# Kernel optimization log

Hardware: AMD Instinct MI355X
Metric: run time of the kernel (lower is better)

The kernel has to match this reference:

```python
import jax, jax.numpy as jnp
import numpy as np

D_MODEL = 1024
N_EXPERTS = 8
TOP_K = 2
D_FF = 4 * D_MODEL
BATCH, SEQ = 4, 2048


def setup_inputs() -> dict:
    key = jax.random.key(0)
    ks = jax.random.split(key, 7)
    s = 0.02
    return {
        "x": jax.random.normal(ks[0], (BATCH, SEQ, D_MODEL), dtype=jnp.float32),
        "Wg": jax.random.normal(ks[1], (D_MODEL, N_EXPERTS), dtype=jnp.float32) * s,
        "bg": jnp.zeros((N_EXPERTS,), dtype=jnp.float32),
        "W1": jax.random.normal(ks[2], (N_EXPERTS, D_MODEL, D_FF), dtype=jnp.float32) * s,
        "b1": jnp.zeros((N_EXPERTS, D_FF), dtype=jnp.float32),
        "W2": jax.random.normal(ks[3], (N_EXPERTS, D_FF, D_MODEL), dtype=jnp.float32) * s,
        "b2": jnp.zeros((N_EXPERTS, D_MODEL), dtype=jnp.float32),
    }


def reference(x, Wg, bg, W1, b1, W2, b2):
    B, S, D = x.shape
    T = B * S
    xf = x.reshape(T, D)  # [T, d_model]

    # Gating: top-k over softmax probabilities
    gate_logits = xf @ Wg + bg                      # [T, E]
    probs = jax.nn.softmax(gate_logits, axis=-1)
    weights, indices = jax.lax.top_k(probs, TOP_K)  # [T, K] each

    # Dense combine weights c[t, e] = sum_k weights[t,k] * (indices[t,k]==e)
    E = Wg.shape[1]
    c = jnp.zeros((T, E), dtype=x.dtype).at[jnp.arange(T)[:, None], indices].add(weights)

    # All-expert FFN as batched GEMMs (same math as masked per-expert loop)
    h = jnp.einsum('td,edf->etf', xf, W1) + b1[:, None, :]   # [E, T, d_ff]
    a = jax.nn.gelu(h, approximate=False)
    y = jnp.einsum('etf,efd->etd', a, W2) + b2[:, None, :]   # [E, T, d_model]

    out = jnp.einsum('te,etd->td', c, y).reshape(B, S, D)
    return out, gate_logits
```

## Files before the change

kernel.cpp:

```cpp
#include <hip/hip_runtime.h>
#include <hip/hip_bf16.h>
#include <math.h>

#define D_MODEL 1024
#define N_EXP   8
#define D_FF    4096
#define T_TOK   8192
#define NPAIR   (T_TOK * 2)
#define CAP_ROWS (NPAIR + N_EXP * 128)
#define MAX_TILES (CAP_ROWS / 128)

typedef __attribute__((ext_vector_type(4)))  float  f32x4;
typedef __attribute__((ext_vector_type(16))) float  f32x16;
typedef __attribute__((ext_vector_type(8)))  __bf16 bf16x8;
typedef __attribute__((ext_vector_type(4)))  __bf16 bf16x4;

#define OFF_W1T   0
#define OFF_W2T   67108864
#define OFF_H     134217728
#define OFF_XR    276824064
#define OFF_META  312475648
#define M_PAIREXP 0
#define M_PAIRW   65536
#define M_ROW2P   131072
#define M_COUNTS  200704
#define M_PADST   200736
#define M_CURSOR  200768
#define M_T2E     201792
#define M_TROW    202336

__device__ __forceinline__ void async_copy16(const void* g, void* s) {
  __builtin_amdgcn_global_load_lds(
      (const __attribute__((address_space(1))) void*)g,
      (__attribute__((address_space(3))) void*)s, 16, 0, 0);
}

__device__ __forceinline__ float gelu_fast(float v) {
  float u = 1.5957691216057308f * (v + 0.044715f * v * v * v);
  return v * __builtin_amdgcn_rcpf(1.f + __expf(-u));
}

__global__ void k_gate(const float* __restrict__ x, const float* __restrict__ Wg,
                       const float* __restrict__ bg, float* __restrict__ logits_out,
                       int* __restrict__ pairExpert, float* __restrict__ pairW) {
  const int t    = blockIdx.x * 4 + (threadIdx.x >> 6);
  const int lane = threadIdx.x & 63;
  const float* xp = x + (size_t)t * D_MODEL;
  float acc[8];
#pragma unroll
  for (int e = 0; e < 8; e++) acc[e] = 0.f;
#pragma unroll
  for (int i = 0; i < 16; i++) {
    int d = i * 64 + lane;
    float xv = xp[d];
    const float4* wr = (const float4*)(Wg + d * 8);
    float4 w0 = wr[0], w1 = wr[1];
    acc[0] += xv * w0.x; acc[1] += xv * w0.y; acc[2] += xv * w0.z; acc[3] += xv * w0.w;
    acc[4] += xv * w1.x; acc[5] += xv * w1.y; acc[6] += xv * w1.z; acc[7] += xv * w1.w;
  }
#pragma unroll
  for (int e = 0; e < 8; e++)
#pragma unroll
    for (int off = 32; off > 0; off >>= 1) acc[e] += __shfl_down(acc[e], off);
  if (lane == 0) {
    float l[8];
#pragma unroll
    for (int e = 0; e < 8; e++) { l[e] = acc[e] + bg[e]; logits_out[t * 8 + e] = l[e]; }
    float m = l[0];
#pragma unroll
    for (int e = 1; e < 8; e++) m = fmaxf(m, l[e]);
    float p[8], s = 0.f;
#pragma unroll
    for (int e = 0; e < 8; e++) { p[e] = expf(l[e] - m); s += p[e]; }
    float inv = 1.0f / s;
    int i1 = 0;
#pragma unroll
    for (int e = 1; e < 8; e++) if (l[e] > l[i1]) i1 = e;
    int i2 = (i1 == 0) ? 1 : 0;
#pragma unroll
    for (int e = 0; e < 8; e++) if (e != i1 && l[e] > l[i2]) i2 = e;
    pairExpert[t * 2 + 0] = i1; pairW[t * 2 + 0] = p[i1] * inv;
    pairExpert[t * 2 + 1] = i2; pairW[t * 2 + 1] = p[i2] * inv;
  }
}

__global__ void k_init(int* __restrict__ row2pair) {
  int i = blockIdx.x * 256 + threadIdx.x;
  if (i < CAP_ROWS) row2pair[i] = -1;
}

__global__ void k_offsets(const int* __restrict__ pairExpert, int* __restrict__ counts,
                          int* __restrict__ padStart, int* __restrict__ cursor,
                          int* __restrict__ t2e, int* __restrict__ trow) {
  __shared__ int hist[8];
  int tid = threadIdx.x;
  if (tid < 8) hist[tid] = 0;
  __syncthreads();
  for (int i = tid; i < NPAIR; i += 256) atomicAdd(&hist[pairExpert[i]], 1);
  __syncthreads();
  if (tid == 0) {
    int run = 0, nt = 0;
    for (int e = 0; e < 8; e++) {
      counts[e] = hist[e]; padStart[e] = run; cursor[e * 32] = 0;
      int tiles = (hist[e] + 127) >> 7;
      for (int i = 0; i < tiles; i++) { t2e[nt] = e; trow[nt] = run + i * 128; nt++; }
      run += tiles * 128;
    }
    for (; nt < MAX_TILES; nt++) t2e[nt] = -1;
  }
}

__global__ void k_place(const int* __restrict__ pairExpert, const int* __restrict__ padStart,
                        int* __restrict__ cursor, int* __restrict__ row2pair) {
  int p = blockIdx.x * 256 + threadIdx.x;
  if (p >= NPAIR) return;
  int e = pairExpert[p];
  int r = atomicAdd(&cursor[e * 32], 1);
  row2pair[padStart[e] + r] = p;
}

__global__ void k_gather(const float* __restrict__ x, const int* __restrict__ row2pair,
                         __bf16* __restrict__ XR) {
  int row = blockIdx.x;
  int pair = row2pair[row];
  int c = threadIdx.x * 4;
  __bf16* dst = XR + (size_t)row * D_MODEL + c;
  if (pair < 0) {
    bf16x4 z = {(__bf16)0.f, (__bf16)0.f, (__bf16)0.f, (__bf16)0.f};
    *(bf16x4*)dst = z;
  } else {
    int t = pair >> 1;
    float4 v = *(const float4*)(x + (size_t)t * D_MODEL + c);
    bf16x4 o = {(__bf16)v.x, (__bf16)v.y, (__bf16)v.z, (__bf16)v.w};
    *(bf16x4*)dst = o;
  }
}

__global__ void k_convT(const float* __restrict__ in, __bf16* __restrict__ out,
                        int R, int C) {
  __shared__ __bf16 tile[64][68];
  int e = blockIdx.z;
  const float* ip = in + (size_t)e * R * C + (size_t)(blockIdx.y * 64) * C + blockIdx.x * 64;
  __bf16* op = out + (size_t)e * R * C + (size_t)(blockIdx.x * 64) * R + blockIdx.y * 64;
#pragma unroll
  for (int it = 0; it < 4; it++) {
    int idx = it * 1024 + threadIdx.x * 4;
    int lr = idx >> 6, lc = idx & 63;
    float4 v = *(const float4*)(ip + (size_t)lr * C + lc);
    bf16x4 o = {(__bf16)v.x, (__bf16)v.y, (__bf16)v.z, (__bf16)v.w};
    *(bf16x4*)&tile[lr][lc] = o;
  }
  __syncthreads();
#pragma unroll
  for (int it = 0; it < 4; it++) {
    int idx = it * 1024 + threadIdx.x * 4;
    int lc = idx >> 6, lr = idx & 63;
    bf16x4 o = {tile[lr + 0][lc], tile[lr + 1][lc], tile[lr + 2][lc], tile[lr + 3][lc]};
    *(bf16x4*)(op + (size_t)lc * R + lr) = o;
  }
}


#define STG(SW, T)                                                         \
  do {                                                                     \
    size_t _ko = (size_t)(T) * 64;                                         \
    async_copy16(srcA0 + _ko, (SW) + w * 1024);                            \
    async_copy16(srcA1 + _ko, (SW) + (w + 4) * 1024);                      \
    async_copy16(srcB0 + _ko, (SW) + 8192 + w * 1024);                     \
    async_copy16(srcB1 + _ko, (SW) + 8192 + (w + 4) * 1024);               \
  } while (0)

#define LDF(SR)                                                            \
  do {                                                                     \
    _Pragma("unroll")                                                      \
    for (int mi = 0; mi < 2; mi++)                                         \
      _Pragma("unroll")                                                    \
      for (int kc = 0; kc < 2; kc++)                                       \
        Af[mi][kc] = *(const bf16x8*)((SR) + (wm + mi * 32 + l31) * 64 + (aoff ^ (kc << 5))); \
    _Pragma("unroll")                                                      \
    for (int nj = 0; nj < 2; nj++)                                         \
      _Pragma("unroll")                                                    \
      for (int kc = 0; kc < 2; kc++)                                       \
        Bf[nj][kc] = *(const bf16x8*)((SR) + 8192 + (wn + nj * 32 + l31) * 64 + (aoff ^ (kc << 5))); \
  } while (0)

#define MFM                                                                \
  do {                                                                     \
    __builtin_amdgcn_s_setprio(1);                                         \
    _Pragma("unroll")                                                      \
    for (int kc = 0; kc < 2; kc++)                                         \
      _Pragma("unroll")                                                    \
      for (int mi = 0; mi < 2; mi++)                                       \
        _Pragma("unroll")                                                  \
        for (int nj = 0; nj < 2; nj++)                                     \
          acc[mi][nj] = __builtin_amdgcn_mfma_f32_32x32x16_bf16(           \
              Af[mi][kc], Bf[nj][kc], acc[mi][nj], 0, 0, 0);               \
    __builtin_amdgcn_s_setprio(0);                                         \
  } while (0)

#define ENDW(N)                                                            \
  do {                                                                     \
    __builtin_amdgcn_sched_barrier(0);                                     \
    asm volatile("s_waitcnt vmcnt(" #N ")" ::: "memory");                  \
    __builtin_amdgcn_s_barrier();                                          \
    asm volatile("" ::: "memory");                                         \
  } while (0)

#define BODY(SR, SW, T) \
  do { bf16x8 Af[2][2], Bf[2][2]; STG(SW, T); LDF(SR); MFM; ENDW(4); } while (0)
#define BODY_N0(SR) \
  do { bf16x8 Af[2][2], Bf[2][2]; LDF(SR); MFM; ENDW(0); } while (0)
#define BODY_LAST(SR) \
  do { bf16x8 Af[2][2], Bf[2][2]; LDF(SR); MFM; } while (0)

__global__ __launch_bounds__(256, 3) void k_gemm1(
    const __bf16* __restrict__ XR, const __bf16* __restrict__ W1T,
    const float* __restrict__ b1, __bf16* __restrict__ H,
    const int* __restrict__ t2e, const int* __restrict__ trow) {
  __shared__ __align__(16) char lds[3][16384];
  const int bid = blockIdx.x;
  const int q = bid >> 8, w8 = bid & 255;
  const int nb = w8 >> 3, mt = q * 8 + (w8 & 7);
  const int e = t2e[mt];
  if (e < 0) return;
  const int rowBase = trow[mt];
  const int n0 = nb * 128;

  const int tid = threadIdx.x;
  const int l = tid & 63, w = tid >> 6;
  const int wm = (w >> 1) * 64, wn = (w & 1) * 64;
  const int l31 = l & 31, half = l >> 5;
  const int rsub = l >> 2;
  const int sg = (l & 3) ^ ((l >> 3) & 3);
  const int aoff = ((half ^ ((l >> 1) & 3)) << 4);

  const char* srcA0 = (const char*)(XR + (size_t)(rowBase + 16 * w + rsub) * D_MODEL) + sg * 16;
  const char* srcA1 = srcA0 + (size_t)64 * D_MODEL * 2;
  const __bf16* Bb = W1T + (size_t)e * D_FF * D_MODEL + (size_t)n0 * D_MODEL;
  const char* srcB0 = (const char*)(Bb + (size_t)(16 * w + rsub) * D_MODEL) + sg * 16;
  const char* srcB1 = srcB0 + (size_t)64 * D_MODEL * 2;

  f32x16 acc[2][2];
#pragma unroll
  for (int i = 0; i < 2; i++)
#pragma unroll
    for (int j = 0; j < 2; j++) acc[i][j] = (f32x16)(0.f);

  char* s0 = &lds[0][0]; char* s1 = &lds[1][0]; char* s2 = &lds[2][0];

  STG(s0, 0);
  STG(s1, 1);
  ENDW(4);

#pragma unroll 1
  for (int g = 0; g < 10; g++) {
    int t = 3 * g;
    BODY(s0, s2, t + 2);
    BODY(s1, s0, t + 3);
    BODY(s2, s1, t + 4);
  }
  BODY_N0(s0);
  BODY_LAST(s1);

  int colv[2]; float biasv[2];
#pragma unroll
  for (int nj = 0; nj < 2; nj++) {
    colv[nj] = n0 + wn + nj * 32 + l31;
    biasv[nj] = b1[e * D_FF + colv[nj]];
  }
#pragma unroll
  for (int mi = 0; mi < 2; mi++)
#pragma unroll
    for (int r = 0; r < 16; r++) {
      size_t row = (size_t)rowBase + wm + mi * 32 + (r & 3) + 8 * (r >> 2) + 4 * half;
#pragma unroll
      for (int nj = 0; nj < 2; nj++)
        H[row * D_FF + colv[nj]] = (__bf16)gelu_fast(acc[mi][nj][r] + biasv[nj]);
    }
}

__global__ __launch_bounds__(256, 3) void k_gemm2(
    const __bf16* __restrict__ H, const __bf16* __restrict__ W2T,
    const float* __restrict__ b2, float* __restrict__ out,
    const int* __restrict__ row2pair, const float* __restrict__ pairW,
    const int* __restrict__ t2e, const int* __restrict__ trow) {
  __shared__ __align__(16) char lds[3][16384];
  const int bid = blockIdx.x;
  const int q = bid >> 6, w8 = bid & 63;
  const int nb = w8 >> 3, mt = q * 8 + (w8 & 7);
  const int e = t2e[mt];
  if (e < 0) return;
  const int rowBase = trow[mt];
  const int n0 = nb * 128;

  const int tid = threadIdx.x;
  const int l = tid & 63, w = tid >> 6;
  const int wm = (w >> 1) * 64, wn = (w & 1) * 64;
  const int l31 = l & 31, half = l >> 5;
  const int rsub = l >> 2;
  const int sg = (l & 3) ^ ((l >> 3) & 3);
  const int aoff = ((half ^ ((l >> 1) & 3)) << 4);

  const char* srcA0 = (const char*)(H + (size_t)(rowBase + 16 * w + rsub) * D_FF) + sg * 16;
  const char* srcA1 = srcA0 + (size_t)64 * D_FF * 2;
  const __bf16* Bb = W2T + (size_t)e * D_MODEL * D_FF + (size_t)n0 * D_FF;
  const char* srcB0 = (const char*)(Bb + (size_t)(16 * w + rsub) * D_FF) + sg * 16;
  const char* srcB1 = srcB0 + (size_t)64 * D_FF * 2;

  f32x16 acc[2][2];
#pragma unroll
  for (int i = 0; i < 2; i++)
#pragma unroll
    for (int j = 0; j < 2; j++) acc[i][j] = (f32x16)(0.f);

  char* s0 = &lds[0][0]; char* s1 = &lds[1][0]; char* s2 = &lds[2][0];

  STG(s0, 0);
  STG(s1, 1);
  ENDW(4);

#pragma unroll 1
  for (int g = 0; g < 42; g++) {
    int t = 3 * g;
    BODY(s0, s2, t + 2);
    BODY(s1, s0, t + 3);
    BODY(s2, s1, t + 4);
  }
  BODY_N0(s0);
  BODY_LAST(s1);

  int colv[2]; float biasv[2];
#pragma unroll
  for (int nj = 0; nj < 2; nj++) {
    colv[nj] = n0 + wn + nj * 32 + l31;
    biasv[nj] = b2[e * D_MODEL + colv[nj]];
  }
#pragma unroll
  for (int mi = 0; mi < 2; mi++)
#pragma unroll
    for (int r = 0; r < 16; r++) {
      int row = rowBase + wm + mi * 32 + (r & 3) + 8 * (r >> 2) + 4 * half;
      int pair = row2pair[row];
      if (pair < 0) continue;
      float pw = pairW[pair];
      size_t tok = (size_t)(pair >> 1);
#pragma unroll
      for (int nj = 0; nj < 2; nj++)
        atomicAdd(out + tok * D_MODEL + colv[nj], pw * (acc[mi][nj][r] + biasv[nj]));
    }
}

extern "C" void kernel_launch(void* const* d_in, const int* in_sizes, int n_in,
                              void* d_out, int out_size, void* d_ws, size_t ws_size,
                              hipStream_t stream) {
  const float* x  = (const float*)d_in[0];
  const float* Wg = (const float*)d_in[1];
  const float* bg = (const float*)d_in[2];
  const float* W1 = (const float*)d_in[3];
  const float* b1 = (const float*)d_in[4];
  const float* W2 = (const float*)d_in[5];
  const float* b2 = (const float*)d_in[6];
  float* out        = (float*)d_out;
  float* logits_out = out + (size_t)T_TOK * D_MODEL;

  char* ws = (char*)d_ws;
  __bf16* W1T = (__bf16*)(ws + OFF_W1T);
  __bf16* W2T = (__bf16*)(ws + OFF_W2T);
  __bf16* H   = (__bf16*)(ws + OFF_H);
  __bf16* XR  = (__bf16*)(ws + OFF_XR);
  char* meta = ws + OFF_META;
  int*   pairExpert = (int*)(meta + M_PAIREXP);
  float* pairW      = (float*)(meta + M_PAIRW);
  int*   row2pair   = (int*)(meta + M_ROW2P);
  int*   counts     = (int*)(meta + M_COUNTS);
  int*   padStart   = (int*)(meta + M_PADST);
  int*   cursor     = (int*)(meta + M_CURSOR);
  int*   t2e        = (int*)(meta + M_T2E);
  int*   trow       = (int*)(meta + M_TROW);

  hipMemsetAsync(out, 0, (size_t)T_TOK * D_MODEL * sizeof(float), stream);

  k_convT<<<dim3(D_FF / 64, D_MODEL / 64, N_EXP), 256, 0, stream>>>(W1, W1T, D_MODEL, D_FF);
  k_convT<<<dim3(D_MODEL / 64, D_FF / 64, N_EXP), 256, 0, stream>>>(W2, W2T, D_FF, D_MODEL);

  k_init<<<(CAP_ROWS + 255) / 256, 256, 0, stream>>>(row2pair);
  k_gate<<<T_TOK / 4, 256, 0, stream>>>(x, Wg, bg, logits_out, pairExpert, pairW);
  k_offsets<<<1, 256, 0, stream>>>(pairExpert, counts, padStart, cursor, t2e, trow);
  k_place<<<NPAIR / 256, 256, 0, stream>>>(pairExpert, padStart, cursor, row2pair);
  k_gather<<<CAP_ROWS, 256, 0, stream>>>(x, row2pair, XR);

  k_gemm1<<<(MAX_TILES / 8) * 256, 256, 0, stream>>>(XR, W1T, b1, H, t2e, trow);
  k_gemm2<<<(MAX_TILES / 8) * 64, 256, 0, stream>>>(H, W2T, b2, out, row2pair, pairW, t2e, trow);
}
```

Measured before the change: 859.7 us.

## Widen expert GEMM tiles to 128x256 with 512 threads and deeper K stages

Both expert GEMMs move from 128x128 tiles with 256 threads to 128x256 tiles with 8 waves. Each stage now loads K=128 into a triple-buffered ~48KB LDS slot, and LDS fragment reads are double-buffered against the MFMAs using lgkmcnt waits. Block-to-tile mapping is changed so consecutive blocks on the same XCD share an M tile. The aim is more reuse of A per block and better hiding of LDS latency. In exchange, occupancy drops to one block per CU and there are more barriers per K stage.

```diff
diff --git a/kernel.cpp b/kernel.cpp
--- a/kernel.cpp
+++ b/kernel.cpp
@@ -9,6 +9,7 @@
 #define NPAIR   (T_TOK * 2)
 #define CAP_ROWS (NPAIR + N_EXP * 128)
 #define MAX_TILES (CAP_ROWS / 128)
+#define SLOT 49152
 
 typedef __attribute__((ext_vector_type(4)))  float  f32x4;
 typedef __attribute__((ext_vector_type(16))) float  f32x16;
@@ -161,84 +162,107 @@
 }
 
 
-#define STG(SW, T)                                                         \
-  do {                                                                     \
-    size_t _ko = (size_t)(T) * 64;                                         \
-    async_copy16(srcA0 + _ko, (SW) + w * 1024);                            \
-    async_copy16(srcA1 + _ko, (SW) + (w + 4) * 1024);                      \
-    async_copy16(srcB0 + _ko, (SW) + 8192 + w * 1024);                     \
-    async_copy16(srcB1 + _ko, (SW) + 8192 + (w + 4) * 1024);               \
-  } while (0)
-
-#define LDF(SR)                                                            \
-  do {                                                                     \
-    _Pragma("unroll")                                                      \
-    for (int mi = 0; mi < 2; mi++)                                         \
-      _Pragma("unroll")                                                    \
-      for (int kc = 0; kc < 2; kc++)                                       \
-        Af[mi][kc] = *(const bf16x8*)((SR) + (wm + mi * 32 + l31) * 64 + (aoff ^ (kc << 5))); \
-    _Pragma("unroll")                                                      \
-    for (int nj = 0; nj < 2; nj++)                                         \
-      _Pragma("unroll")                                                    \
-      for (int kc = 0; kc < 2; kc++)                                       \
-        Bf[nj][kc] = *(const bf16x8*)((SR) + 8192 + (wn + nj * 32 + l31) * 64 + (aoff ^ (kc << 5))); \
-  } while (0)
-
-#define MFM                                                                \
+template <int NT>
+__device__ __forceinline__ void gemm_core(const char* gA, const char* gB,
+                                          char* lds0, int w, bool wlow,
+                                          int offA0, int offB0,
+                                          f32x16 (&acc)[2][2]) {
+#define STG_KQ(P, KB, SW)                                                  \
+  do {                                                                     \
+    if (wlow) async_copy16(gA + (KB) + (P) * 32,                           \
+                           (SW) + (P) * 4096 + w * 1024);                  \
+    async_copy16(gB + (KB) + (P) * 32,                                     \
+                 (SW) + 16384 + (P) * 8192 + w * 1024);                    \
+  } while (0)
+#define RDF(A0, A1, B0, B1, RB, KC)                                        \
+  do {                                                                     \
+    A0 = *(const bf16x8*)((RB) + (KC) * 4096 + offA0);                     \
+    A1 = *(const bf16x8*)((RB) + (KC) * 4096 + offA0 + 1024);              \
+    B0 = *(const bf16x8*)((RB) + 16384 + (KC) * 8192 + offB0);             \
+    B1 = *(const bf16x8*)((RB) + 16384 + (KC) * 8192 + offB0 + 1024);      \
+  } while (0)
+#define MM4(A0, A1, B0, B1)                                                \
   do {                                                                     \
     __builtin_amdgcn_s_setprio(1);                                         \
-    _Pragma("unroll")                                                      \
-    for (int kc = 0; kc < 2; kc++)                                         \
-      _Pragma("unroll")                                                    \
-      for (int mi = 0; mi < 2; mi++)                                       \
-        _Pragma("unroll")                                                  \
-        for (int nj = 0; nj < 2; nj++)                                     \
-          acc[mi][nj] = __builtin_amdgcn_mfma_f32_32x32x16_bf16(           \
-              Af[mi][kc], Bf[nj][kc], acc[mi][nj], 0, 0, 0);               \
+    acc[0][0] = __builtin_amdgcn_mfma_f32_32x32x16_bf16(A0, B0, acc[0][0], 0, 0, 0); \
+    acc[0][1] = __builtin_amdgcn_mfma_f32_32x32x16_bf16(A0, B1, acc[0][1], 0, 0, 0); \
+    acc[1][0] = __builtin_amdgcn_mfma_f32_32x32x16_bf16(A1, B0, acc[1][0], 0, 0, 0); \
+    acc[1][1] = __builtin_amdgcn_mfma_f32_32x32x16_bf16(A1, B1, acc[1][1], 0, 0, 0); \
     __builtin_amdgcn_s_setprio(0);                                         \
   } while (0)
-
-#define ENDW(N)                                                            \
-  do {                                                                     \
-    __builtin_amdgcn_sched_barrier(0);                                     \
-    asm volatile("s_waitcnt vmcnt(" #N ")" ::: "memory");                  \
+#define WBAR                                                               \
+  do {                                                                     \
+    if (wlow) asm volatile("s_waitcnt vmcnt(12)" ::: "memory");            \
+    else      asm volatile("s_waitcnt vmcnt(6)" ::: "memory");             \
     __builtin_amdgcn_s_barrier();                                          \
     asm volatile("" ::: "memory");                                         \
   } while (0)
-
-#define BODY(SR, SW, T) \
-  do { bf16x8 Af[2][2], Bf[2][2]; STG(SW, T); LDF(SR); MFM; ENDW(4); } while (0)
-#define BODY_N0(SR) \
-  do { bf16x8 Af[2][2], Bf[2][2]; LDF(SR); MFM; ENDW(0); } while (0)
-#define BODY_LAST(SR) \
-  do { bf16x8 Af[2][2], Bf[2][2]; LDF(SR); MFM; } while (0)
-
-__global__ __launch_bounds__(256, 3) void k_gemm1(
+#define LG4                                                                \
+  do {                                                                     \
+    asm volatile("s_waitcnt lgkmcnt(4)" ::: "memory");                     \
+    __builtin_amdgcn_sched_barrier(0);                                     \
+  } while (0)
+
+  bf16x8 F0a0, F0a1, F0b0, F0b1, F1a0, F1a1, F1b0, F1b1;
+  const char* p0 = lds0;
+  const char* p1 = lds0 + SLOT;
+  const char* p2 = lds0 + 2 * SLOT;
+
+#pragma unroll
+  for (int p = 0; p < 4; p++) STG_KQ(p, 0, lds0);
+#pragma unroll
+  for (int p = 0; p < 4; p++) STG_KQ(p, 128, lds0 + SLOT);
+  WBAR;
+  RDF(F0a0, F0a1, F0b0, F0b1, p0, 0);
+
+#pragma unroll 1
+  for (int t = 0; t < NT; t++) {
+    char* wb = (char*)p2;
+    const size_t kb = (size_t)((t + 2 < NT) ? t + 2 : NT - 1) * 128;
+    STG_KQ(0, kb, wb); RDF(F1a0, F1a1, F1b0, F1b1, p0, 1); LG4;
+    MM4(F0a0, F0a1, F0b0, F0b1); WBAR;
+    STG_KQ(1, kb, wb); RDF(F0a0, F0a1, F0b0, F0b1, p0, 2); LG4;
+    MM4(F1a0, F1a1, F1b0, F1b1); WBAR;
+    STG_KQ(2, kb, wb); RDF(F1a0, F1a1, F1b0, F1b1, p0, 3); LG4;
+    MM4(F0a0, F0a1, F0b0, F0b1); WBAR;
+    STG_KQ(3, kb, wb); RDF(F0a0, F0a1, F0b0, F0b1, p1, 0); LG4;
+    MM4(F1a0, F1a1, F1b0, F1b1); WBAR;
+    const char* tp = p0; p0 = p1; p1 = p2; p2 = tp;
+  }
+#undef STG_KQ
+#undef RDF
+#undef MM4
+#undef WBAR
+#undef LG4
+}
+
+__global__ __launch_bounds__(512, 1) void k_gemm1(
     const __bf16* __restrict__ XR, const __bf16* __restrict__ W1T,
     const float* __restrict__ b1, __bf16* __restrict__ H,
     const int* __restrict__ t2e, const int* __restrict__ trow) {
-  __shared__ __align__(16) char lds[3][16384];
+  __shared__ __align__(16) char lds[3 * SLOT];
   const int bid = blockIdx.x;
-  const int q = bid >> 8, w8 = bid & 255;
-  const int nb = w8 >> 3, mt = q * 8 + (w8 & 7);
+  const int xcd = bid & 7, q = bid >> 3;
+  const int nb = q & 15;
+  const int mt = (q >> 4) * 8 + xcd;
   const int e = t2e[mt];
   if (e < 0) return;
   const int rowBase = trow[mt];
-  const int n0 = nb * 128;
+  const int n0 = nb * 256;
 
   const int tid = threadIdx.x;
   const int l = tid & 63, w = tid >> 6;
-  const int wm = (w >> 1) * 64, wn = (w & 1) * 64;
-  const int l31 = l & 31, half = l >> 5;
-  const int rsub = l >> 2;
-  const int sg = (l & 3) ^ ((l >> 3) & 3);
-  const int aoff = ((half ^ ((l >> 1) & 3)) << 4);
-
-  const char* srcA0 = (const char*)(XR + (size_t)(rowBase + 16 * w + rsub) * D_MODEL) + sg * 16;
-  const char* srcA1 = srcA0 + (size_t)64 * D_MODEL * 2;
-  const __bf16* Bb = W1T + (size_t)e * D_FF * D_MODEL + (size_t)n0 * D_MODEL;
-  const char* srcB0 = (const char*)(Bb + (size_t)(16 * w + rsub) * D_MODEL) + sg * 16;
-  const char* srcB1 = srcB0 + (size_t)64 * D_MODEL * 2;
+  const bool wlow = w < 4;
+  const int wm = (w >> 2) * 64, wn = (w & 3) * 64;
+  const int l31 = l & 31, h = l >> 5;
+  const int hg = (l & 1) ^ ((l >> 3) & 1);
+  const int rowA0 = wm + l31, rowB0 = wn + l31;
+  const int offA0 = rowA0 * 32 + ((h ^ ((rowA0 >> 2) & 1)) << 4);
+  const int offB0 = rowB0 * 32 + ((h ^ ((rowB0 >> 2) & 1)) << 4);
+
+  const char* gA = (const char*)(XR + (size_t)(rowBase + 32 * w + (l >> 1)) * D_MODEL) + hg * 16;
+  const char* gB = (const char*)(W1T + (size_t)e * D_FF * D_MODEL
+                                 + (size_t)(n0 + 32 * w + (l >> 1)) * D_MODEL) + hg * 16;
 
   f32x16 acc[2][2];
 #pragma unroll
@@ -246,21 +270,7 @@
 #pragma unroll
     for (int j = 0; j < 2; j++) acc[i][j] = (f32x16)(0.f);
 
-  char* s0 = &lds[0][0]; char* s1 = &lds[1][0]; char* s2 = &lds[2][0];
-
-  STG(s0, 0);
-  STG(s1, 1);
-  ENDW(4);
-
-#pragma unroll 1
-  for (int g = 0; g < 10; g++) {
-    int t = 3 * g;
-    BODY(s0, s2, t + 2);
-    BODY(s1, s0, t + 3);
-    BODY(s2, s1, t + 4);
-  }
-  BODY_N0(s0);
-  BODY_LAST(s1);
+  gemm_core<16>(gA, gB, lds, w, wlow, offA0, offB0, acc);
 
   int colv[2]; float biasv[2];
 #pragma unroll
@@ -272,40 +282,41 @@
   for (int mi = 0; mi < 2; mi++)
 #pragma unroll
     for (int r = 0; r < 16; r++) {
-      size_t row = (size_t)rowBase + wm + mi * 32 + (r & 3) + 8 * (r >> 2) + 4 * half;
+      size_t row = (size_t)rowBase + wm + mi * 32 + (r & 3) + 8 * (r >> 2) + 4 * h;
 #pragma unroll
       for (int nj = 0; nj < 2; nj++)
         H[row * D_FF + colv[nj]] = (__bf16)gelu_fast(acc[mi][nj][r] + biasv[nj]);
     }
 }
 
-__global__ __launch_bounds__(256, 3) void k_gemm2(
+__global__ __launch_bounds__(512, 1) void k_gemm2(
     const __bf16* __restrict__ H, const __bf16* __restrict__ W2T,
     const float* __restrict__ b2, float* __restrict__ out,
     const int* __restrict__ row2pair, const float* __restrict__ pairW,
     const int* __restrict__ t2e, const int* __restrict__ trow) {
-  __shared__ __align__(16) char lds[3][16384];
+  __shared__ __align__(16) char lds[3 * SLOT];
   const int bid = blockIdx.x;
-  const int q = bid >> 6, w8 = bid & 63;
-  const int nb = w8 >> 3, mt = q * 8 + (w8 & 7);
+  const int xcd = bid & 7, q = bid >> 3;
+  const int nb = q & 3;
+  const int mt = (q >> 2) * 8 + xcd;
   const int e = t2e[mt];
   if (e < 0) return;
   const int rowBase = trow[mt];
-  const int n0 = nb * 128;
+  const int n0 = nb * 256;
 
   const int tid = threadIdx.x;
   const int l = tid & 63, w = tid >> 6;
-  const int wm = (w >> 1) * 64, wn = (w & 1) * 64;
-  const int l31 = l & 31, half = l >> 5;
-  const int rsub = l >> 2;
-  const int sg = (l & 3) ^ ((l >> 3) & 3);
-  const int aoff = ((half ^ ((l >> 1) & 3)) << 4);
-
-  const char* srcA0 = (const char*)(H + (size_t)(rowBase + 16 * w + rsub) * D_FF) + sg * 16;
-  const char* srcA1 = srcA0 + (size_t)64 * D_FF * 2;
-  const __bf16* Bb = W2T + (size_t)e * D_MODEL * D_FF + (size_t)n0 * D_FF;
-  const char* srcB0 = (const char*)(Bb + (size_t)(16 * w + rsub) * D_FF) + sg * 16;
-  const char* srcB1 = srcB0 + (size_t)64 * D_FF * 2;
+  const bool wlow = w < 4;
+  const int wm = (w >> 2) * 64, wn = (w & 3) * 64;
+  const int l31 = l & 31, h = l >> 5;
+  const int hg = (l & 1) ^ ((l >> 3) & 1);
+  const int rowA0 = wm + l31, rowB0 = wn + l31;
+  const int offA0 = rowA0 * 32 + ((h ^ ((rowA0 >> 2) & 1)) << 4);
+  const int offB0 = rowB0 * 32 + ((h ^ ((rowB0 >> 2) & 1)) << 4);
+
+  const char* gA = (const char*)(H + (size_t)(rowBase + 32 * w + (l >> 1)) * D_FF) + hg * 16;
+  const char* gB = (const char*)(W2T + (size_t)e * D_MODEL * D_FF
+                                 + (size_t)(n0 + 32 * w + (l >> 1)) * D_FF) + hg * 16;
 
   f32x16 acc[2][2];
 #pragma unroll
@@ -313,21 +324,7 @@
 #pragma unroll
     for (int j = 0; j < 2; j++) acc[i][j] = (f32x16)(0.f);
 
-  char* s0 = &lds[0][0]; char* s1 = &lds[1][0]; char* s2 = &lds[2][0];
-
-  STG(s0, 0);
-  STG(s1, 1);
-  ENDW(4);
-
-#pragma unroll 1
-  for (int g = 0; g < 42; g++) {
-    int t = 3 * g;
-    BODY(s0, s2, t + 2);
-    BODY(s1, s0, t + 3);
-    BODY(s2, s1, t + 4);
-  }
-  BODY_N0(s0);
-  BODY_LAST(s1);
+  gemm_core<64>(gA, gB, lds, w, wlow, offA0, offB0, acc);
 
   int colv[2]; float biasv[2];
 #pragma unroll
@@ -339,7 +336,7 @@
   for (int mi = 0; mi < 2; mi++)
 #pragma unroll
     for (int r = 0; r < 16; r++) {
-      int row = rowBase + wm + mi * 32 + (r & 3) + 8 * (r >> 2) + 4 * half;
+      int row = rowBase + wm + mi * 32 + (r & 3) + 8 * (r >> 2) + 4 * h;
       int pair = row2pair[row];
       if (pair < 0) continue;
       float pw = pairW[pair];
@@ -389,6 +386,6 @@
   k_place<<<NPAIR / 256, 256, 0, stream>>>(pairExpert, padStart, cursor, row2pair);
   k_gather<<<CAP_ROWS, 256, 0, stream>>>(x, row2pair, XR);
 
-  k_gemm1<<<(MAX_TILES / 8) * 256, 256, 0, stream>>>(XR, W1T, b1, H, t2e, trow);
-  k_gemm2<<<(MAX_TILES / 8) * 64, 256, 0, stream>>>(H, W2T, b2, out, row2pair, pairW, t2e, trow);
-}
+  k_gemm1<<<MAX_TILES * 16, 512, 0, stream>>>(XR, W1T, b1, H, t2e, trow);
+  k_gemm2<<<MAX_TILES * 4, 512, 0, stream>>>(H, W2T, b2, out, row2pair, pairW, t2e, trow);
+}
```

Result: slower. 1.067 ms (+24.2%).
